# Kernel tuning notes

Measured on AMD Instinct MI355X. Metric: run time of the kernel, lower is better.

Reference implementation:

```python
import jax, jax.numpy as jnp
import numpy as np

K_CURV = 1.0   # manifold curvature k
KERNEL = 5
STRIDE = 1
PAD = 2


def setup_inputs() -> dict:
    key = jax.random.key(0)
    k1, k2, k3 = jax.random.split(key, 3)
    bsz, L, Cin, Cout = 16, 8192, 64, 64
    # Build points on the Lorentz manifold: time = sqrt(||space||^2 + k)
    space = jax.random.normal(k1, (bsz, L, Cin - 1), dtype=jnp.float32)
    time = jnp.sqrt(jnp.sum(space ** 2, axis=-1, keepdims=True) + K_CURV)
    x = jnp.concatenate([time, space], axis=-1)  # (bs, len, Cin)
    lin_feat = (Cin - 1) * KERNEL + 1            # 316
    W = jax.random.normal(k2, (Cout, lin_feat), dtype=jnp.float32) / np.sqrt(lin_feat).astype(np.float32)
    b = jax.random.normal(k3, (Cout,), dtype=jnp.float32) * 0.01
    return {"x": x, "W": W, "b": b}


def reference(x, W, b):
    bsz, L, C = x.shape
    sqrt_k = jnp.sqrt(jnp.asarray(K_CURV, x.dtype))
    # pad along length, then clamp time component to sqrt(k) (F.pad + clamp_)
    xp = jnp.pad(x, ((0, 0), (PAD, PAD), (0, 0)))
    xp = xp.at[..., 0].set(jnp.maximum(xp[..., 0], sqrt_k))
    L_out = (L + 2 * PAD - KERNEL) // STRIDE + 1
    # unfold(1, K, stride): gather overlapping windows -> (bs, L_out, K, C)
    idx = jnp.arange(L_out)[:, None] * STRIDE + jnp.arange(KERNEL)[None, :]
    patches = xp[:, idx, :]
    patches = jnp.swapaxes(patches, 2, 3)        # (bs, L_out, C, K) as torch unfold
    # Lorentz time rescale over the K time coords of each patch
    p_time = patches[:, :, 0, :]                 # (bs, L_out, K)
    t_resc = jnp.sqrt(jnp.sum(p_time ** 2, axis=-1, keepdims=True)
                      - (KERNEL - 1) * K_CURV)   # (bs, L_out, 1)
    p_space = patches[:, :, 1:, :].reshape(bsz, L_out, -1)  # (bs, L_out, (C-1)*K)
    feats = jnp.concatenate([t_resc, p_space], axis=-1)     # (bs, L_out, lin_feat)
    # LorentzFullyConnected: linear, then recompute time from space norm
    y = jnp.einsum('blf,of->blo', feats, W) + b              # (bs, L_out, Cout)
    y_space = y[..., 1:]
    y_time = jnp.sqrt(jnp.sum(y_space ** 2, axis=-1, keepdims=True) + K_CURV)
    return jnp.concatenate([y_time, y_space], axis=-1)
```

## Files before the change

### kernel.cpp

```cpp
#include <hip/hip_runtime.h>
#include <math.h>


#define BSZ   16
#define LLEN  8192
#define CIN   64
#define COUT  64
#define KW    5
#define LINF  316
#define MTILE 64
#define ROWS  68
#define ASTR  72
#define KB    320
#define TPB   2
#define NTILES (BSZ * LLEN / MTILE)
#define GRID   (NTILES / TPB)

typedef __attribute__((ext_vector_type(8))) short  short8;
typedef __attribute__((ext_vector_type(4))) float  float4v;

__device__ inline unsigned short f2bf(float f) {
    unsigned u = __builtin_bit_cast(unsigned int, f);
    u += 0x7FFFu + ((u >> 16) & 1u);
    return (unsigned short)(u >> 16);
}

__global__ __launch_bounds__(256) void prep_W(const float* __restrict__ W,
                                              unsigned short* __restrict__ Wb) {
    int i = blockIdx.x * 256 + threadIdx.x;
    if (i >= COUT * KB) return;
    int n   = i / KB;
    int kk  = i - n * KB;
    int tap = kk >> 6;
    int c   = kk & 63;
    float v = (c == 0) ? 0.f : W[n * LINF + 1 + (c - 1) * KW + tap];
    Wb[i] = f2bf(v);
}

__global__ __launch_bounds__(256, 3) void lorentz_mfma(
    const float* __restrict__ x, const unsigned short* __restrict__ Wb,
    const float* __restrict__ W, const float* __restrict__ bias,
    float* __restrict__ out)
{
    __shared__ unsigned short At[2][ROWS * ASTR];
    __shared__ float tcol[2][72];
    __shared__ float pss[2][2][64];

    int tid  = threadIdx.x;
    int lane = tid & 63;
    int wv   = tid >> 6;
    int col  = lane & 15, quad = lane >> 4;
    int nhalf = wv & 1;
    int mbase = (wv >> 1) * 32;

    int tile0 = blockIdx.x * TPB;

    short8 breg[2][10];
    #pragma unroll
    for (int j = 0; j < 2; ++j) {
        const unsigned short* bp = Wb + (nhalf * 32 + j * 16 + col) * KB + quad * 8;
        #pragma unroll
        for (int kk = 0; kk < 10; ++kk)
            breg[j][kk] = *(const short8*)(bp + kk * 32);
    }
    float bo[2], w0[2];
    #pragma unroll
    for (int j = 0; j < 2; ++j) {
        int n = nhalf * 32 + j * 16 + col;
        bo[j] = bias[n];
        w0[j] = W[n * LINF];
    }

    float4 sreg[5];
    bool   sin[5];

    auto stage_load = [&](int tile) {
        int b  = tile >> 7;
        int l0 = (tile & 127) * MTILE;
        const float* xb = x + ((size_t)b * LLEN) * CIN;
        #pragma unroll
        for (int itc = 0; itc < 5; ++itc) {
            int i = tid + itc * 256;
            if (i < ROWS * 16) {
                int r = i >> 4, ch = i & 15;
                int row = l0 - 2 + r;
                sin[itc] = (row >= 0) && (row < LLEN);
                int rowc = min(max(row, 0), LLEN - 1);
                sreg[itc] = ((const float4*)(xb + (size_t)rowc * CIN))[ch];
            }
        }
    };
    auto stage_write = [&](int nb) {
        #pragma unroll
        for (int itc = 0; itc < 5; ++itc) {
            int i = tid + itc * 256;
            if (i < ROWS * 16) {
                int r = i >> 4, ch = i & 15;
                float4 v = sreg[itc];
                if (!sin[itc]) { v.x = (ch == 0) ? 1.f : 0.f; v.y = 0.f; v.z = 0.f; v.w = 0.f; }
                if (ch == 0) tcol[nb][r] = v.x;
                ushort4 pk;
                pk.x = f2bf(v.x); pk.y = f2bf(v.y); pk.z = f2bf(v.z); pk.w = f2bf(v.w);
                *(ushort4*)&At[nb][r * ASTR + ch * 4] = pk;
            }
        }
    };

    stage_load(tile0);
    stage_write(0);
    __syncthreads();

    int cur = 0;
    #pragma unroll
    for (int it = 0; it < TPB; ++it) {
        int tile = tile0 + it;
        bool more = (it + 1 < TPB);
        if (more) stage_load(tile + 1);

        float4v acc[2][2];
        #pragma unroll
        for (int ms = 0; ms < 2; ++ms)
            #pragma unroll
            for (int j = 0; j < 2; ++j)
                acc[ms][j] = (float4v){0.f, 0.f, 0.f, 0.f};
        #pragma unroll
        for (int kk = 0; kk < 10; ++kk) {
            int tap = kk >> 1, ks = kk & 1;
            #pragma unroll
            for (int ms = 0; ms < 2; ++ms) {
                short8 afr = *(const short8*)&At[cur][(mbase + ms * 16 + col + tap) * ASTR
                                                     + ks * 32 + quad * 8];
                acc[ms][0] = __builtin_amdgcn_mfma_f32_16x16x32_bf16(afr, breg[0][kk], acc[ms][0], 0, 0, 0);
                acc[ms][1] = __builtin_amdgcn_mfma_f32_16x16x32_bf16(afr, breg[1][kk], acc[ms][1], 0, 0, 0);
            }
        }

        float trs[2][4];
        #pragma unroll
        for (int ms = 0; ms < 2; ++ms) {
            int p0 = mbase + ms * 16 + quad * 4;
            float4 a = *(const float4*)&tcol[cur][p0];
            float4 c = *(const float4*)&tcol[cur][p0 + 4];
            float tw[8] = {a.x, a.y, a.z, a.w, c.x, c.y, c.z, c.w};
            #pragma unroll
            for (int reg = 0; reg < 4; ++reg) {
                float s = 0.f;
                #pragma unroll
                for (int t = 0; t < KW; ++t) { float v = tw[reg + t]; s += v * v; }
                trs[ms][reg] = sqrtf(s - (float)(KW - 1));
            }
        }

        float y[2][2][4];
        float sq[2][4];
        #pragma unroll
        for (int ms = 0; ms < 2; ++ms)
            #pragma unroll
            for (int reg = 0; reg < 4; ++reg) {
                float s = 0.f;
                #pragma unroll
                for (int j = 0; j < 2; ++j) {
                    float v = acc[ms][j][reg] + bo[j] + trs[ms][reg] * w0[j];
                    y[ms][j][reg] = v;
                    bool isc0 = (nhalf == 0) && (j == 0) && (col == 0);
                    s += isc0 ? 0.f : v * v;
                }
                sq[ms][reg] = s;
            }
        #pragma unroll
        for (int ms = 0; ms < 2; ++ms)
            #pragma unroll
            for (int reg = 0; reg < 4; ++reg) {
                #pragma unroll
                for (int msk = 1; msk < 16; msk <<= 1)
                    sq[ms][reg] += __shfl_xor(sq[ms][reg], msk, 64);
                if (col == 0)
                    pss[cur][nhalf][mbase + ms * 16 + quad * 4 + reg] = sq[ms][reg];
            }

        if (more) stage_write(cur ^ 1);
        __syncthreads();

        #pragma unroll
        for (int ms = 0; ms < 2; ++ms)
            #pragma unroll
            for (int reg = 0; reg < 4; ++reg) {
                int row = mbase + ms * 16 + quad * 4 + reg;
                float tot = sq[ms][reg] + pss[cur][1 ^ nhalf][row];
                if (nhalf == 0 && col == 0)
                    y[ms][0][reg] = sqrtf(tot + 1.f);
                float* orow = out + ((size_t)tile * MTILE + row) * COUT + nhalf * 32 + col;
                orow[0]  = y[ms][0][reg];
                orow[16] = y[ms][1][reg];
            }
        cur ^= 1;
    }
}

extern "C" void kernel_launch(void* const* d_in, const int* in_sizes, int n_in,
                              void* d_out, int out_size, void* d_ws, size_t ws_size,
                              hipStream_t stream) {
    const float* x    = (const float*)d_in[0];
    const float* W    = (const float*)d_in[1];
    const float* bias = (const float*)d_in[2];
    float* out = (float*)d_out;
    unsigned short* Wb = (unsigned short*)d_ws;

    hipLaunchKernelGGL(prep_W, dim3((COUT * KB + 255) / 256), dim3(256), 0, stream,
                       W, Wb);
    hipLaunchKernelGGL(lorentz_mfma, dim3(GRID), dim3(256), 0, stream,
                       x, Wb, W, bias, out);
}
```

Measured before the change: 100.3 us.

## Fuse weight bf16 conversion into main kernel, use DPP row sums, larger TPB

```diff
diff --git a/kernel.cpp b/kernel.cpp
--- a/kernel.cpp
+++ b/kernel.cpp
@@ -11,8 +11,7 @@
 #define MTILE 64
 #define ROWS  68
 #define ASTR  72
-#define KB    320
-#define TPB   2
+#define TPB   4
 #define NTILES (BSZ * LLEN / MTILE)
 #define GRID   (NTILES / TPB)
 
@@ -25,22 +24,24 @@
     return (unsigned short)(u >> 16);
 }
 
-__global__ __launch_bounds__(256) void prep_W(const float* __restrict__ W,
-                                              unsigned short* __restrict__ Wb) {
-    int i = blockIdx.x * 256 + threadIdx.x;
-    if (i >= COUT * KB) return;
-    int n   = i / KB;
-    int kk  = i - n * KB;
-    int tap = kk >> 6;
-    int c   = kk & 63;
-    float v = (c == 0) ? 0.f : W[n * LINF + 1 + (c - 1) * KW + tap];
-    Wb[i] = f2bf(v);
-}
-
-__global__ __launch_bounds__(256, 3) void lorentz_mfma(
-    const float* __restrict__ x, const unsigned short* __restrict__ Wb,
-    const float* __restrict__ W, const float* __restrict__ bias,
-    float* __restrict__ out)
+template <int CTRL>
+__device__ inline float dpp_add(float v) {
+    int x = __builtin_bit_cast(int, v);
+    int t = __builtin_amdgcn_update_dpp(0, x, CTRL, 0xF, 0xF, true);
+    return v + __builtin_bit_cast(float, t);
+}
+
+__device__ inline float dpp_rowsum16_hi(float v) {
+    v = dpp_add<0x111>(v);
+    v = dpp_add<0x112>(v);
+    v = dpp_add<0x114>(v);
+    v = dpp_add<0x118>(v);
+    return v;
+}
+
+__global__ __launch_bounds__(256) void lorentz_mfma(
+    const float* __restrict__ x, const float* __restrict__ W,
+    const float* __restrict__ bias, float* __restrict__ out)
 {
     __shared__ unsigned short At[2][ROWS * ASTR];
     __shared__ float tcol[2][72];
@@ -54,22 +55,6 @@
     int mbase = (wv >> 1) * 32;
 
     int tile0 = blockIdx.x * TPB;
-
-    short8 breg[2][10];
-    #pragma unroll
-    for (int j = 0; j < 2; ++j) {
-        const unsigned short* bp = Wb + (nhalf * 32 + j * 16 + col) * KB + quad * 8;
-        #pragma unroll
-        for (int kk = 0; kk < 10; ++kk)
-            breg[j][kk] = *(const short8*)(bp + kk * 32);
-    }
-    float bo[2], w0[2];
-    #pragma unroll
-    for (int j = 0; j < 2; ++j) {
-        int n = nhalf * 32 + j * 16 + col;
-        bo[j] = bias[n];
-        w0[j] = W[n * LINF];
-    }
 
     float4 sreg[5];
     bool   sin[5];
@@ -107,6 +92,29 @@
     };
 
     stage_load(tile0);
+
+    short8 breg[2][10];
+    float bo[2], w0[2];
+    #pragma unroll
+    for (int j = 0; j < 2; ++j) {
+        int n = nhalf * 32 + j * 16 + col;
+        const float* wrow = W + (size_t)n * LINF;
+        #pragma unroll
+        for (int kk = 0; kk < 10; ++kk) {
+            int tap = kk >> 1, ks = kk & 1;
+            short8 t;
+            #pragma unroll
+            for (int e = 0; e < 8; ++e) {
+                int c = ks * 32 + quad * 8 + e;
+                float v = (c == 0) ? 0.f : wrow[1 + (c - 1) * KW + tap];
+                t[e] = (short)f2bf(v);
+            }
+            breg[j][kk] = t;
+        }
+        bo[j] = bias[n];
+        w0[j] = wrow[0];
+    }
+
     stage_write(0);
     __syncthreads();
 
@@ -171,11 +179,9 @@
         for (int ms = 0; ms < 2; ++ms)
             #pragma unroll
             for (int reg = 0; reg < 4; ++reg) {
-                #pragma unroll
-                for (int msk = 1; msk < 16; msk <<= 1)
-                    sq[ms][reg] += __shfl_xor(sq[ms][reg], msk, 64);
-                if (col == 0)
-                    pss[cur][nhalf][mbase + ms * 16 + quad * 4 + reg] = sq[ms][reg];
+                float rs = dpp_rowsum16_hi(sq[ms][reg]);
+                if (col == 15)
+                    pss[cur][nhalf][mbase + ms * 16 + quad * 4 + reg] = rs;
             }
 
         if (more) stage_write(cur ^ 1);
@@ -186,9 +192,10 @@
             #pragma unroll
             for (int reg = 0; reg < 4; ++reg) {
                 int row = mbase + ms * 16 + quad * 4 + reg;
-                float tot = sq[ms][reg] + pss[cur][1 ^ nhalf][row];
-                if (nhalf == 0 && col == 0)
+                if (nhalf == 0 && col == 0) {
+                    float tot = pss[cur][0][row] + pss[cur][1][row];
                     y[ms][0][reg] = sqrtf(tot + 1.f);
+                }
                 float* orow = out + ((size_t)tile * MTILE + row) * COUT + nhalf * 32 + col;
                 orow[0]  = y[ms][0][reg];
                 orow[16] = y[ms][1][reg];
@@ -204,10 +211,7 @@
     const float* W    = (const float*)d_in[1];
     const float* bias = (const float*)d_in[2];
     float* out = (float*)d_out;
-    unsigned short* Wb = (unsigned short*)d_ws;
-
-    hipLaunchKernelGGL(prep_W, dim3((COUT * KB + 255) / 256), dim3(256), 0, stream,
-                       W, Wb);
+
     hipLaunchKernelGGL(lorentz_mfma, dim3(GRID), dim3(256), 0, stream,
-                       x, Wb, W, bias, out);
-}
+                       x, W, bias, out);
+}
```

Result: slower. 124.5 us (+24.1%).

## Give each wave a 16-column output slice and reduce row norms with DPP

Applied to the files above, without the earlier changes.

```diff
diff --git a/kernel.cpp b/kernel.cpp
--- a/kernel.cpp
+++ b/kernel.cpp
@@ -25,6 +25,21 @@
     return (unsigned short)(u >> 16);
 }
 
+template <int CTRL>
+__device__ inline float dpp_add(float v) {
+    int x = __builtin_bit_cast(int, v);
+    int t = __builtin_amdgcn_update_dpp(0, x, CTRL, 0xF, 0xF, true);
+    return v + __builtin_bit_cast(float, t);
+}
+
+__device__ inline float dpp_rowsum16_hi(float v) {
+    v = dpp_add<0x111>(v);
+    v = dpp_add<0x112>(v);
+    v = dpp_add<0x114>(v);
+    v = dpp_add<0x118>(v);
+    return v;
+}
+
 __global__ __launch_bounds__(256) void prep_W(const float* __restrict__ W,
                                               unsigned short* __restrict__ Wb) {
     int i = blockIdx.x * 256 + threadIdx.x;
@@ -37,39 +52,22 @@
     Wb[i] = f2bf(v);
 }
 
-__global__ __launch_bounds__(256, 3) void lorentz_mfma(
+__global__ __launch_bounds__(256, 4) void lorentz_mfma(
     const float* __restrict__ x, const unsigned short* __restrict__ Wb,
     const float* __restrict__ W, const float* __restrict__ bias,
     float* __restrict__ out)
 {
     __shared__ unsigned short At[2][ROWS * ASTR];
     __shared__ float tcol[2][72];
-    __shared__ float pss[2][2][64];
+    __shared__ float pss[2][4][64];
 
     int tid  = threadIdx.x;
     int lane = tid & 63;
-    int wv   = tid >> 6;
+    int nq   = tid >> 6;
     int col  = lane & 15, quad = lane >> 4;
-    int nhalf = wv & 1;
-    int mbase = (wv >> 1) * 32;
+    int n    = nq * 16 + col;
 
     int tile0 = blockIdx.x * TPB;
-
-    short8 breg[2][10];
-    #pragma unroll
-    for (int j = 0; j < 2; ++j) {
-        const unsigned short* bp = Wb + (nhalf * 32 + j * 16 + col) * KB + quad * 8;
-        #pragma unroll
-        for (int kk = 0; kk < 10; ++kk)
-            breg[j][kk] = *(const short8*)(bp + kk * 32);
-    }
-    float bo[2], w0[2];
-    #pragma unroll
-    for (int j = 0; j < 2; ++j) {
-        int n = nhalf * 32 + j * 16 + col;
-        bo[j] = bias[n];
-        w0[j] = W[n * LINF];
-    }
 
     float4 sreg[5];
     bool   sin[5];
@@ -107,6 +105,17 @@
     };
 
     stage_load(tile0);
+
+    short8 breg[10];
+    {
+        const unsigned short* bp = Wb + (size_t)n * KB + quad * 8;
+        #pragma unroll
+        for (int kk = 0; kk < 10; ++kk)
+            breg[kk] = *(const short8*)(bp + kk * 32);
+    }
+    float bo = bias[n];
+    float w0 = W[(size_t)n * LINF];
+
     stage_write(0);
     __syncthreads();
 
@@ -117,82 +126,63 @@
         bool more = (it + 1 < TPB);
         if (more) stage_load(tile + 1);
 
-        float4v acc[2][2];
-        #pragma unroll
-        for (int ms = 0; ms < 2; ++ms)
-            #pragma unroll
-            for (int j = 0; j < 2; ++j)
-                acc[ms][j] = (float4v){0.f, 0.f, 0.f, 0.f};
+        float4v acc[4];
+        #pragma unroll
+        for (int ms = 0; ms < 4; ++ms) acc[ms] = (float4v){0.f, 0.f, 0.f, 0.f};
         #pragma unroll
         for (int kk = 0; kk < 10; ++kk) {
             int tap = kk >> 1, ks = kk & 1;
             #pragma unroll
-            for (int ms = 0; ms < 2; ++ms) {
-                short8 afr = *(const short8*)&At[cur][(mbase + ms * 16 + col + tap) * ASTR
+            for (int ms = 0; ms < 4; ++ms) {
+                short8 afr = *(const short8*)&At[cur][(ms * 16 + col + tap) * ASTR
                                                      + ks * 32 + quad * 8];
-                acc[ms][0] = __builtin_amdgcn_mfma_f32_16x16x32_bf16(afr, breg[0][kk], acc[ms][0], 0, 0, 0);
-                acc[ms][1] = __builtin_amdgcn_mfma_f32_16x16x32_bf16(afr, breg[1][kk], acc[ms][1], 0, 0, 0);
-            }
-        }
-
-        float trs[2][4];
-        #pragma unroll
-        for (int ms = 0; ms < 2; ++ms) {
-            int p0 = mbase + ms * 16 + quad * 4;
+                acc[ms] = __builtin_amdgcn_mfma_f32_16x16x32_bf16(afr, breg[kk], acc[ms], 0, 0, 0);
+            }
+        }
+
+        #pragma unroll
+        for (int ms = 0; ms < 4; ++ms) {
+            int p0 = ms * 16 + quad * 4;
             float4 a = *(const float4*)&tcol[cur][p0];
             float4 c = *(const float4*)&tcol[cur][p0 + 4];
             float tw[8] = {a.x, a.y, a.z, a.w, c.x, c.y, c.z, c.w};
+            float sq[4];
             #pragma unroll
             for (int reg = 0; reg < 4; ++reg) {
                 float s = 0.f;
                 #pragma unroll
                 for (int t = 0; t < KW; ++t) { float v = tw[reg + t]; s += v * v; }
-                trs[ms][reg] = sqrtf(s - (float)(KW - 1));
-            }
-        }
-
-        float y[2][2][4];
-        float sq[2][4];
-        #pragma unroll
-        for (int ms = 0; ms < 2; ++ms)
+                float trs = sqrtf(s - (float)(KW - 1));
+                float v = acc[ms][reg] + bo + trs * w0;
+                acc[ms][reg] = v;
+                bool isc0 = (nq == 0) && (col == 0);
+                sq[reg] = isc0 ? 0.f : v * v;
+            }
             #pragma unroll
             for (int reg = 0; reg < 4; ++reg) {
-                float s = 0.f;
-                #pragma unroll
-                for (int j = 0; j < 2; ++j) {
-                    float v = acc[ms][j][reg] + bo[j] + trs[ms][reg] * w0[j];
-                    y[ms][j][reg] = v;
-                    bool isc0 = (nhalf == 0) && (j == 0) && (col == 0);
-                    s += isc0 ? 0.f : v * v;
-                }
-                sq[ms][reg] = s;
-            }
-        #pragma unroll
-        for (int ms = 0; ms < 2; ++ms)
-            #pragma unroll
-            for (int reg = 0; reg < 4; ++reg) {
-                #pragma unroll
-                for (int msk = 1; msk < 16; msk <<= 1)
-                    sq[ms][reg] += __shfl_xor(sq[ms][reg], msk, 64);
-                if (col == 0)
-                    pss[cur][nhalf][mbase + ms * 16 + quad * 4 + reg] = sq[ms][reg];
-            }
+                float rs = dpp_rowsum16_hi(sq[reg]);
+                if (col == 15)
+                    pss[cur][nq][ms * 16 + quad * 4 + reg] = rs;
+            }
+        }
 
         if (more) stage_write(cur ^ 1);
         __syncthreads();
 
         #pragma unroll
-        for (int ms = 0; ms < 2; ++ms)
+        for (int ms = 0; ms < 4; ++ms) {
             #pragma unroll
             for (int reg = 0; reg < 4; ++reg) {
-                int row = mbase + ms * 16 + quad * 4 + reg;
-                float tot = sq[ms][reg] + pss[cur][1 ^ nhalf][row];
-                if (nhalf == 0 && col == 0)
-                    y[ms][0][reg] = sqrtf(tot + 1.f);
-                float* orow = out + ((size_t)tile * MTILE + row) * COUT + nhalf * 32 + col;
-                orow[0]  = y[ms][0][reg];
-                orow[16] = y[ms][1][reg];
-            }
+                int row = ms * 16 + quad * 4 + reg;
+                float v = acc[ms][reg];
+                if (nq == 0 && col == 0) {
+                    float tot = pss[cur][0][row] + pss[cur][1][row]
+                              + pss[cur][2][row] + pss[cur][3][row];
+                    v = sqrtf(tot + 1.f);
+                }
+                out[((size_t)tile * MTILE + row) * COUT + n] = v;
+            }
+        }
         cur ^= 1;
     }
 }
```

Result: faster. 98.03 us (-2.2%).
